# Optimization experiments

Measured on AMD Instinct MI355X. Metric: run time of the kernel, lower is better.

The kernel has to match this reference:

```python
import jax, jax.numpy as jnp
import numpy as np
import math

L, B, S, D, H, FF = 6, 4, 1024, 1024, 16, 4096
HD = D // H
EPS = 1e-5


def _ln(x, g, b):
    m = jnp.mean(x, axis=-1, keepdims=True)
    v = jnp.mean(jnp.square(x - m), axis=-1, keepdims=True)
    return (x - m) / jnp.sqrt(v + EPS) * g + b


def setup_inputs() -> dict:
    key = jax.random.key(0)
    ks = jax.random.split(key, 8)
    std = 0.02
    inp = {
        'x': jax.random.normal(ks[0], (B, S, D), jnp.float32),
        'lengths': jax.random.randint(ks[1], (B,), S // 2, S + 1),
        'rel_bias': jax.random.normal(ks[2], (H, S, S), jnp.float32) * std,
        'ln1_g': jnp.ones((L, D), jnp.float32),
        'ln1_b': jnp.zeros((L, D), jnp.float32),
        'qkv_w': jax.random.normal(ks[3], (L, D, 3 * D), jnp.float32) * std,
        'qkv_b': jnp.zeros((L, 3 * D), jnp.float32),
        'out_w': jax.random.normal(ks[4], (L, D, D), jnp.float32) * std,
        'out_b': jnp.zeros((L, D), jnp.float32),
        'ln2_g': jnp.ones((L, D), jnp.float32),
        'ln2_b': jnp.zeros((L, D), jnp.float32),
        'fc1_w': jax.random.normal(ks[5], (L, D, FF), jnp.float32) * std,
        'fc1_b': jnp.zeros((L, FF), jnp.float32),
        'fc2_w': jax.random.normal(ks[6], (L, FF, D), jnp.float32) * std,
        'fc2_b': jnp.zeros((L, D), jnp.float32),
    }
    return inp


def reference(x, lengths, rel_bias, ln1_g, ln1_b, qkv_w, qkv_b, out_w, out_b,
              ln2_g, ln2_b, fc1_w, fc1_b, fc2_w, fc2_b):
    # causal additive mask [S,S]: -inf above the diagonal (torch.triu diagonal=1)
    ar = jnp.arange(S)
    causal = jnp.where(ar[None, :] > ar[:, None], -jnp.inf, 0.0).astype(x.dtype)
    # key padding mask [B,S]: True where position is padding
    pad = ar[None, :] >= lengths[:, None]
    scale = 1.0 / math.sqrt(HD)

    for i in range(L):
        # --- attention sub-block (pre-LN) ---
        xn = _ln(x, ln1_g[i], ln1_b[i])
        qkv = xn @ qkv_w[i] + qkv_b[i]                      # [B,S,3D]
        q, k, v = jnp.split(qkv, 3, axis=-1)
        q = q.reshape(B, S, H, HD)
        k = k.reshape(B, S, H, HD)
        v = v.reshape(B, S, H, HD)
        scores = jnp.einsum('bqhd,bkhd->bhqk', q, k) * scale  # [B,H,S,S]
        scores = scores + rel_bias[None] + causal[None, None]
        scores = jnp.where(pad[:, None, None, :], -jnp.inf, scores)
        attn = jax.nn.softmax(scores, axis=-1)
        o = jnp.einsum('bhqk,bkhd->bqhd', attn, v).reshape(B, S, D)
        o = o @ out_w[i] + out_b[i]
        o = jnp.where(pad[:, :, None], 0.0, o)
        x = x + o
        # --- feed-forward sub-block (LN inside FF, residual outside) ---
        h = _ln(x, ln2_g[i], ln2_b[i])
        h = jax.nn.gelu(h @ fc1_w[i] + fc1_b[i], approximate=False)
        h = h @ fc2_w[i] + fc2_b[i]
        x = x + h
    return x
```

## Files before the change

kernel.cpp:

```cpp
#include <hip/hip_runtime.h>
#include <cstdint>
#include <cstddef>

constexpr int L_ = 6, B_ = 4, S_ = 1024, D_ = 1024, H_ = 16, FF_ = 4096;
constexpr int D3_ = 3 * D_;
constexpr int HD_ = D_ / H_;

typedef float f32x4 __attribute__((ext_vector_type(4)));
typedef __bf16 bf16x8 __attribute__((ext_vector_type(8)));
typedef unsigned short u16;
typedef u16 u16x4 __attribute__((ext_vector_type(4)));
typedef u16 u16x8 __attribute__((ext_vector_type(8)));

__device__ __forceinline__ u16 f2bf(float f) {
    union { float f; uint32_t u; } v; v.f = f;
    uint32_t r = v.u + 0x7FFFu + ((v.u >> 16) & 1u);
    return (u16)(r >> 16);
}
__device__ __forceinline__ float bf2f(u16 u) {
    union { uint32_t u; float f; } v; v.u = ((uint32_t)u) << 16;
    return v.f;
}

__device__ __forceinline__ void gload16(const void* g, void* l) {
    __builtin_amdgcn_global_load_lds(
        (const __attribute__((address_space(1))) unsigned int*)g,
        (__attribute__((address_space(3))) unsigned int*)l,
        16, 0, 0);
}

__global__ __launch_bounds__(256) void cvt_bias(
    const float* __restrict__ src, u16* __restrict__ dst)
{
    size_t i = ((size_t)blockIdx.x * 256 + threadIdx.x) * 8;
    f32x4 a = *(const f32x4*)(src + i);
    f32x4 b = *(const f32x4*)(src + i + 4);
    u16x8 o;
    #pragma unroll
    for (int r = 0; r < 4; ++r) { o[r] = f2bf(a[r]); o[4 + r] = f2bf(b[r]); }
    *(u16x8*)(dst + i) = o;
}

__global__ __launch_bounds__(256) void cvt_layer(
    const float* __restrict__ qw, const float* __restrict__ ow,
    const float* __restrict__ f1w, const float* __restrict__ f2w,
    u16* __restrict__ tq, u16* __restrict__ to,
    u16* __restrict__ t1, u16* __restrict__ t2)
{
    __shared__ float tile[64][65];
    const int bid = blockIdx.x, tid = threadIdx.x;
    const float* W; u16* WT; int K, N, bn, bk;
    if (bid < 768)       { W = qw;  WT = tq; K = 1024; N = 3072; int t = bid;        bn = (t % 48) * 64; bk = (t / 48) * 64; }
    else if (bid < 1024) { W = ow;  WT = to; K = 1024; N = 1024; int t = bid - 768;  bn = (t % 16) * 64; bk = (t / 16) * 64; }
    else if (bid < 2048) { W = f1w; WT = t1; K = 1024; N = 4096; int t = bid - 1024; bn = (t % 64) * 64; bk = (t / 64) * 64; }
    else                 { W = f2w; WT = t2; K = 4096; N = 1024; int t = bid - 2048; bn = (t % 16) * 64; bk = (t / 16) * 64; }
    #pragma unroll
    for (int i = 0; i < 16; ++i) {
        int idx = i * 256 + tid;
        int r = idx >> 6, c = idx & 63;
        tile[r][c] = W[(size_t)(bk + r) * N + bn + c];
    }
    __syncthreads();
    #pragma unroll
    for (int i = 0; i < 16; ++i) {
        int idx = i * 256 + tid;
        int r = idx >> 6, c = idx & 63;
        WT[(size_t)(bn + r) * K + bk + c] = f2bf(tile[c][r]);
    }
}

__global__ __launch_bounds__(256) void ln_kernel(
    const float* __restrict__ X, const float* __restrict__ g,
    const float* __restrict__ bp, u16* __restrict__ out)
{
    const int row = blockIdx.x, tid = threadIdx.x;
    const float* xr = X + (size_t)row * D_;
    f32x4 v = *(const f32x4*)(xr + tid * 4);
    float s  = v[0] + v[1] + v[2] + v[3];
    float s2 = v[0]*v[0] + v[1]*v[1] + v[2]*v[2] + v[3]*v[3];
    #pragma unroll
    for (int off = 32; off >= 1; off >>= 1) {
        s  += __shfl_down(s,  off);
        s2 += __shfl_down(s2, off);
    }
    __shared__ float red[8];
    const int lane = tid & 63, wid = tid >> 6;
    if (lane == 0) { red[wid] = s; red[4 + wid] = s2; }
    __syncthreads();
    s  = red[0] + red[1] + red[2] + red[3];
    s2 = red[4] + red[5] + red[6] + red[7];
    float mean = s * (1.f / D_);
    float var  = s2 * (1.f / D_) - mean * mean;
    float rstd = rsqrtf(var + 1e-5f);
    f32x4 gv = *(const f32x4*)(g  + tid * 4);
    f32x4 bv = *(const f32x4*)(bp + tid * 4);
    u16x4 o4;
    #pragma unroll
    for (int r = 0; r < 4; ++r) o4[r] = f2bf((v[r] - mean) * rstd * gv[r] + bv[r]);
    *(u16x4*)(out + (size_t)row * D_ + tid * 4) = o4;
}

template<int MODE>
__global__ __launch_bounds__(256, 2) void gemmk(
    const u16* __restrict__ A, const u16* __restrict__ BT,
    const float* __restrict__ bias,
    u16* __restrict__ Cb, float* __restrict__ X, u16* __restrict__ VT,
    const int* __restrict__ lengths,
    int M, int N, int K)
{
    __shared__ __align__(16) char sb0[24576];
    __shared__ __align__(16) char sb1[24576];
    __shared__ __align__(16) char sb2[24576];

    const int tid = threadIdx.x;
    const int lane = tid & 63;
    const int w = tid >> 6;
    const int grp = lane >> 4, l15 = lane & 15;
    const int wm = w >> 1, wn = w & 1;

    const int gx = gridDim.x, gy = gridDim.y;
    const int nwg = gx * gy * gridDim.z;
    int lid = blockIdx.x + gx * (blockIdx.y + gy * blockIdx.z);
    {
        int q = nwg >> 3, r = nwg & 7;
        int xcd = lid & 7, wi = lid >> 3;
        lid = (xcd < r ? xcd * (q + 1) : r * (q + 1) + (xcd - r) * q) + wi;
    }
    const int bx = lid % gx;
    const int byz = lid / gx;
    const int by = byz % gy, bz = byz / gy;

    const int m0 = by * 256, n0 = bx * 128;
    const int Kh = K / gridDim.z;
    const int k0 = bz * Kh;
    const int NT = Kh >> 5;

    const int lrow = lane >> 2;
    const int cchunk = (lane & 3) ^ ((lane >> 3) & 3);
    const u16* gA = A  + (size_t)(m0 + w * 64 + lrow) * K + k0 + cchunk * 8;
    const u16* gB = BT + (size_t)(n0 + w * 32 + lrow) * K + k0 + cchunk * 8;
    const size_t row16 = (size_t)16 * K;
    const int rslot = (grp ^ ((l15 >> 1) & 3)) * 16;

#define STAGE(t, BUF) do {                                                    \
        const u16* pa_ = gA + (size_t)(t) * 32;                               \
        const u16* pb_ = gB + (size_t)(t) * 32;                               \
        char* la_ = (BUF) + w * 4096;                                         \
        char* lb_ = (BUF) + 16384 + w * 2048;                                 \
        gload16(pa_,              la_);                                       \
        gload16(pa_ + row16,      la_ + 1024);                                \
        gload16(pa_ + 2 * row16,  la_ + 2048);                                \
        gload16(pa_ + 3 * row16,  la_ + 3072);                                \
        gload16(pb_,              lb_);                                       \
        gload16(pb_ + row16,      lb_ + 1024); } while (0)

    f32x4 acc[8][4] = {};

    STAGE(0, sb0);
    if (NT > 1) STAGE(1, sb1);
    char* bA = sb0; char* bB = sb1; char* bC = sb2;

    for (int t = 0; t < NT; ++t) {
        if (t + 1 < NT) asm volatile("s_waitcnt vmcnt(6)" ::: "memory");
        else            asm volatile("s_waitcnt vmcnt(0)" ::: "memory");
        __builtin_amdgcn_s_barrier();
        if (t + 2 < NT) STAGE(t + 2, bC);

        const char* Ab = bA;
        const char* Bb = bA + 16384;
        bf16x8 bfr[4], af[8];
        #pragma unroll
        for (int nf = 0; nf < 4; ++nf)
            bfr[nf] = *(const bf16x8*)(Bb + (wn * 64 + nf * 16 + l15) * 64 + rslot);
        #pragma unroll
        for (int mf = 0; mf < 8; ++mf)
            af[mf] = *(const bf16x8*)(Ab + (wm * 128 + mf * 16 + l15) * 64 + rslot);
        __builtin_amdgcn_s_setprio(1);
        #pragma unroll
        for (int mf = 0; mf < 8; ++mf)
            #pragma unroll
            for (int nf = 0; nf < 4; ++nf)
                acc[mf][nf] = __builtin_amdgcn_mfma_f32_16x16x32_bf16(
                    af[mf], bfr[nf], acc[mf][nf], 0, 0, 0);
        __builtin_amdgcn_s_setprio(0);

        char* tmp = bA; bA = bB; bB = bC; bC = tmp;
    }
#undef STAGE

    const float bscale = (k0 == 0) ? 1.f : 0.f;
    #pragma unroll
    for (int mi = 0; mi < 8; ++mi) {
        int row_g = m0 + wm * 128 + mi * 16 + grp * 4;
        #pragma unroll
        for (int nf = 0; nf < 4; ++nf) {
            int col_g = n0 + wn * 64 + nf * 16 + l15;
            float bv = bias[col_g] * bscale;
            f32x4 v = acc[mi][nf];
            if constexpr (MODE == 0) {
                if (col_g < 2 * D_) {
                    #pragma unroll
                    for (int r = 0; r < 4; ++r)
                        Cb[(size_t)(row_g + r) * N + col_g] = f2bf(v[r] + bv);
                } else {
                    u16x4 o4;
                    #pragma unroll
                    for (int r = 0; r < 4; ++r) o4[r] = f2bf(v[r] + bv);
                    int vrow = ((row_g >> 10) << 10) + (col_g - 2 * D_);
                    *(u16x4*)(VT + (size_t)vrow * S_ + (row_g & 1023)) = o4;
                }
            } else if constexpr (MODE == 2) {
                #pragma unroll
                for (int r = 0; r < 4; ++r) {
                    float tv = v[r] + bv;
                    float ge = 0.5f * tv * (1.f + erff(tv * 0.70710678118654752f));
                    Cb[(size_t)(row_g + r) * N + col_g] = f2bf(ge);
                }
            } else if constexpr (MODE == 1) {
                int len = lengths[row_g >> 10];
                #pragma unroll
                for (int r = 0; r < 4; ++r) {
                    int row = row_g + r;
                    float add = ((row & 1023) >= len) ? 0.f : (v[r] + bv);
                    atomicAdd(&X[(size_t)row * N + col_g], add);
                }
            } else {
                #pragma unroll
                for (int r = 0; r < 4; ++r)
                    atomicAdd(&X[(size_t)(row_g + r) * N + col_g], v[r] + bv);
            }
        }
    }
}

__global__ __launch_bounds__(256) void attn_kernel(
    const u16* __restrict__ qkv,
    const u16* __restrict__ vt,
    const u16* __restrict__ rbb,
    const int* __restrict__ lengths,
    u16* __restrict__ obuf)
{
    __shared__ __align__(16) char kls[64 * 128];
    __shared__ __align__(16) char vls[64 * 128];
    const int tid = threadIdx.x, lane = tid & 63, wid = tid >> 6;
    const int grp = lane >> 4, l15 = lane & 15;
    const int bh = blockIdx.x, qt = blockIdx.y;
    const int b = bh >> 4, h = bh & 15;
    const int len = lengths[b];
    const int qrow = qt * 64 + wid * 16 + l15;

    bf16x8 qf[2];
    {
        const u16* qp = qkv + ((size_t)(b * S_ + qrow)) * D3_ + h * 64 + grp * 8;
        qf[0] = *(const bf16x8*)qp;
        qf[1] = *(const bf16x8*)(qp + 32);
    }
    f32x4 oacc[4] = {};
    float m_run = -INFINITY, lsum = 0.f;
    int kt_end = (len + 63) >> 6;
    if (qt + 1 < kt_end) kt_end = qt + 1;

    for (int kt = 0; kt < kt_end; ++kt) {
        __syncthreads();
        #pragma unroll
        for (int i = 0; i < 2; ++i) {
            int id2 = tid + i * 256;
            int r = id2 >> 3, gg = id2 & 7;
            int sw = (r & 7) << 4;
            bf16x8 kv = *(const bf16x8*)(qkv + ((size_t)(b * S_ + kt * 64 + r)) * D3_ + D_ + h * 64 + gg * 8);
            *(bf16x8*)(kls + r * 128 + ((gg * 16) ^ sw)) = kv;
            bf16x8 vv = *(const bf16x8*)(vt + ((size_t)(bh * 64 + r)) * S_ + kt * 64 + gg * 8);
            *(bf16x8*)(vls + r * 128 + ((gg * 16) ^ sw)) = vv;
        }
        __syncthreads();

        f32x4 sf[4] = {};
        #pragma unroll
        for (int f = 0; f < 4; ++f) {
            int r = f * 16 + l15;
            int sw = (r & 7) << 4;
            #pragma unroll
            for (int t = 0; t < 2; ++t) {
                bf16x8 af = *(const bf16x8*)(kls + r * 128 + (((t * 32 + grp * 8) * 2) ^ sw));
                sf[f] = __builtin_amdgcn_mfma_f32_16x16x32_bf16(af, qf[t], sf[f], 0, 0, 0);
            }
        }
        float p[4][4];
        float tmax = -INFINITY;
        #pragma unroll
        for (int f = 0; f < 4; ++f) {
            u16x4 bi = *(const u16x4*)(rbb + ((size_t)h * S_ + qrow) * S_ + kt * 64 + f * 16 + grp * 4);
            #pragma unroll
            for (int r = 0; r < 4; ++r) {
                int kp = kt * 64 + f * 16 + grp * 4 + r;
                bool valid = (kp <= qrow) && (kp < len);
                float sv = valid ? fmaf(sf[f][r], 0.125f, bf2f(bi[r])) : -INFINITY;
                p[f][r] = sv;
                tmax = fmaxf(tmax, sv);
            }
        }
        tmax = fmaxf(tmax, __shfl_xor(tmax, 16));
        tmax = fmaxf(tmax, __shfl_xor(tmax, 32));
        float m_new = fmaxf(m_run, tmax);
        float alpha = expf(m_run - m_new);
        float psum = 0.f;
        #pragma unroll
        for (int f = 0; f < 4; ++f)
            #pragma unroll
            for (int r = 0; r < 4; ++r) {
                float e = expf(p[f][r] - m_new);
                p[f][r] = e; psum += e;
            }
        psum += __shfl_xor(psum, 16);
        psum += __shfl_xor(psum, 32);
        lsum = lsum * alpha + psum;
        m_run = m_new;
        #pragma unroll
        for (int fo = 0; fo < 4; ++fo) {
            oacc[fo][0] *= alpha; oacc[fo][1] *= alpha;
            oacc[fo][2] *= alpha; oacc[fo][3] *= alpha;
        }
        #pragma unroll
        for (int t = 0; t < 2; ++t) {
            union { u16 u[8]; bf16x8 v; } pb;
            #pragma unroll
            for (int j = 0; j < 4; ++j) {
                pb.u[j]     = f2bf(p[2 * t][j]);
                pb.u[4 + j] = f2bf(p[2 * t + 1][j]);
            }
            #pragma unroll
            for (int fo = 0; fo < 4; ++fo) {
                int r = fo * 16 + l15;
                int sw = (r & 7) << 4;
                union { u16x4 h4[2]; bf16x8 v; } av;
                av.h4[0] = *(const u16x4*)(vls + r * 128 + ((t * 64 + grp * 8)      ^ sw));
                av.h4[1] = *(const u16x4*)(vls + r * 128 + ((t * 64 + grp * 8 + 32) ^ sw));
                oacc[fo] = __builtin_amdgcn_mfma_f32_16x16x32_bf16(av.v, pb.v, oacc[fo], 0, 0, 0);
            }
        }
    }
    float inv = 1.f / lsum;
    #pragma unroll
    for (int fo = 0; fo < 4; ++fo)
        #pragma unroll
        for (int r = 0; r < 4; ++r) {
            int hd = fo * 16 + grp * 4 + r;
            obuf[((size_t)(b * S_) + qrow) * D_ + h * 64 + hd] = f2bf(oacc[fo][r] * inv);
        }
}

extern "C" void kernel_launch(void* const* d_in, const int* in_sizes, int n_in,
                              void* d_out, int out_size, void* d_ws, size_t ws_size,
                              hipStream_t stream)
{
    const float* x_in     = (const float*)d_in[0];
    const int*   lengths  = (const int*)d_in[1];
    const float* rel_bias = (const float*)d_in[2];
    const float* ln1_g    = (const float*)d_in[3];
    const float* ln1_b    = (const float*)d_in[4];
    const float* qkv_w    = (const float*)d_in[5];
    const float* qkv_b    = (const float*)d_in[6];
    const float* out_w    = (const float*)d_in[7];
    const float* out_b    = (const float*)d_in[8];
    const float* ln2_g    = (const float*)d_in[9];
    const float* ln2_b    = (const float*)d_in[10];
    const float* fc1_w    = (const float*)d_in[11];
    const float* fc1_b    = (const float*)d_in[12];
    const float* fc2_w    = (const float*)d_in[13];
    const float* fc2_b    = (const float*)d_in[14];
    float* X = (float*)d_out;

    char* ws = (char*)d_ws;
    size_t off = 0;
    auto alloc = [&](size_t bytes) {
        char* p = ws + off;
        off = (off + bytes + 255) & ~(size_t)255;
        return p;
    };
    u16* wT_qkv = (u16*)alloc((size_t)D3_ * D_ * 2);
    u16* wT_out = (u16*)alloc((size_t)D_ * D_ * 2);
    u16* wT_fc1 = (u16*)alloc((size_t)FF_ * D_ * 2);
    u16* wT_fc2 = (u16*)alloc((size_t)D_ * FF_ * 2);
    u16* xn     = (u16*)alloc((size_t)B_ * S_ * D_ * 2);
    u16* qkvb   = (u16*)alloc((size_t)B_ * S_ * D3_ * 2);
    u16* vtb    = (u16*)alloc((size_t)B_ * H_ * HD_ * S_ * 2);
    u16* ob     = (u16*)alloc((size_t)B_ * S_ * D_ * 2);
    u16* h1     = (u16*)alloc((size_t)B_ * S_ * FF_ * 2);
    u16* rbb    = (u16*)alloc((size_t)H_ * S_ * S_ * 2);

    const int M = B_ * S_;

    hipMemcpyAsync(X, x_in, (size_t)M * D_ * sizeof(float),
                   hipMemcpyDeviceToDevice, stream);
    cvt_bias<<<(H_ * S_ * S_) / (256 * 8), 256, 0, stream>>>(rel_bias, rbb);

    for (int i = 0; i < L_; ++i) {
        cvt_layer<<<3072, 256, 0, stream>>>(
            qkv_w + (size_t)i * D_ * D3_, out_w + (size_t)i * D_ * D_,
            fc1_w + (size_t)i * D_ * FF_, fc2_w + (size_t)i * FF_ * D_,
            wT_qkv, wT_out, wT_fc1, wT_fc2);

        ln_kernel<<<M, 256, 0, stream>>>(X, ln1_g + i * D_, ln1_b + i * D_, xn);
        gemmk<0><<<dim3(D3_ / 128, M / 256, 1), 256, 0, stream>>>(
            xn, wT_qkv, qkv_b + (size_t)i * D3_, qkvb, nullptr, vtb, nullptr, M, D3_, D_);
        attn_kernel<<<dim3(B_ * H_, S_ / 64), 256, 0, stream>>>(
            qkvb, vtb, rbb, lengths, ob);
        gemmk<1><<<dim3(D_ / 128, M / 256, 4), 256, 0, stream>>>(
            ob, wT_out, out_b + (size_t)i * D_, nullptr, X, nullptr, lengths, M, D_, D_);

        ln_kernel<<<M, 256, 0, stream>>>(X, ln2_g + i * D_, ln2_b + i * D_, xn);
        gemmk<2><<<dim3(FF_ / 128, M / 256, 1), 256, 0, stream>>>(
            xn, wT_fc1, fc1_b + (size_t)i * FF_, h1, nullptr, nullptr, nullptr, M, FF_, D_);
        gemmk<3><<<dim3(D_ / 128, M / 256, 4), 256, 0, stream>>>(
            h1, wT_fc2, fc2_b + (size_t)i * D_, nullptr, X, nullptr, nullptr, M, D_, FF_);
    }
}
```

Before: 1.962 ms.

## Replace triple-buffered 256x128 GEMM with single-buffer 128x128 tile kernel

Swaps the 256x128 GEMM, which used a triple-buffered LDS pipeline and async gloads, for a simpler 128x128 tile kernel. The new kernel loads one K-slice per iteration with two syncthreads barriers and has no prefetch. Grid sizes change to match, and the out-projection split-K drops from 4 to 2. The aim is more workgroups per GEMM, but the change gives up load/compute overlap and halves per-tile data reuse.

```diff
diff --git a/kernel.cpp b/kernel.cpp
--- a/kernel.cpp
+++ b/kernel.cpp
@@ -101,22 +101,20 @@
 }
 
 template<int MODE>
-__global__ __launch_bounds__(256, 2) void gemmk(
+__global__ __launch_bounds__(256) void gemm128(
     const u16* __restrict__ A, const u16* __restrict__ BT,
     const float* __restrict__ bias,
     u16* __restrict__ Cb, float* __restrict__ X, u16* __restrict__ VT,
     const int* __restrict__ lengths,
     int M, int N, int K)
 {
-    __shared__ __align__(16) char sb0[24576];
-    __shared__ __align__(16) char sb1[24576];
-    __shared__ __align__(16) char sb2[24576];
-
+    __shared__ __align__(16) u16 lA[128 * 32];
+    __shared__ __align__(16) u16 lB[128 * 32];
     const int tid = threadIdx.x;
     const int lane = tid & 63;
-    const int w = tid >> 6;
     const int grp = lane >> 4, l15 = lane & 15;
-    const int wm = w >> 1, wn = w & 1;
+    const int wid = tid >> 6;
+    const int wm = wid >> 1, wn = wid & 1;
 
     const int gx = gridDim.x, gy = gridDim.y;
     const int nwg = gx * gy * gridDim.z;
@@ -130,73 +128,55 @@
     const int byz = lid / gx;
     const int by = byz % gy, bz = byz / gy;
 
-    const int m0 = by * 256, n0 = bx * 128;
+    const int m0 = by * 128, n0 = bx * 128;
     const int Kh = K / gridDim.z;
     const int k0 = bz * Kh;
-    const int NT = Kh >> 5;
 
     const int lrow = lane >> 2;
     const int cchunk = (lane & 3) ^ ((lane >> 3) & 3);
-    const u16* gA = A  + (size_t)(m0 + w * 64 + lrow) * K + k0 + cchunk * 8;
-    const u16* gB = BT + (size_t)(n0 + w * 32 + lrow) * K + k0 + cchunk * 8;
-    const size_t row16 = (size_t)16 * K;
+    const u16* gA = A  + (size_t)(m0 + wid * 32 + lrow) * K + k0 + cchunk * 8;
+    const u16* gB = BT + (size_t)(n0 + wid * 32 + lrow) * K + k0 + cchunk * 8;
+    char* lAw = (char*)lA + wid * 2048;
+    char* lBw = (char*)lB + wid * 2048;
+    const size_t rstep = (size_t)16 * K;
+
     const int rslot = (grp ^ ((l15 >> 1) & 3)) * 16;
 
-#define STAGE(t, BUF) do {                                                    \
-        const u16* pa_ = gA + (size_t)(t) * 32;                               \
-        const u16* pb_ = gB + (size_t)(t) * 32;                               \
-        char* la_ = (BUF) + w * 4096;                                         \
-        char* lb_ = (BUF) + 16384 + w * 2048;                                 \
-        gload16(pa_,              la_);                                       \
-        gload16(pa_ + row16,      la_ + 1024);                                \
-        gload16(pa_ + 2 * row16,  la_ + 2048);                                \
-        gload16(pa_ + 3 * row16,  la_ + 3072);                                \
-        gload16(pb_,              lb_);                                       \
-        gload16(pb_ + row16,      lb_ + 1024); } while (0)
-
-    f32x4 acc[8][4] = {};
-
-    STAGE(0, sb0);
-    if (NT > 1) STAGE(1, sb1);
-    char* bA = sb0; char* bB = sb1; char* bC = sb2;
-
-    for (int t = 0; t < NT; ++t) {
-        if (t + 1 < NT) asm volatile("s_waitcnt vmcnt(6)" ::: "memory");
-        else            asm volatile("s_waitcnt vmcnt(0)" ::: "memory");
-        __builtin_amdgcn_s_barrier();
-        if (t + 2 < NT) STAGE(t + 2, bC);
-
-        const char* Ab = bA;
-        const char* Bb = bA + 16384;
-        bf16x8 bfr[4], af[8];
-        #pragma unroll
-        for (int nf = 0; nf < 4; ++nf)
-            bfr[nf] = *(const bf16x8*)(Bb + (wn * 64 + nf * 16 + l15) * 64 + rslot);
-        #pragma unroll
-        for (int mf = 0; mf < 8; ++mf)
-            af[mf] = *(const bf16x8*)(Ab + (wm * 128 + mf * 16 + l15) * 64 + rslot);
-        __builtin_amdgcn_s_setprio(1);
-        #pragma unroll
-        for (int mf = 0; mf < 8; ++mf)
+    f32x4 acc[4][4] = {};
+    for (int kk = 0; kk < Kh; kk += 32) {
+        gload16(gA + kk,         lAw);
+        gload16(gA + kk + rstep, lAw + 1024);
+        gload16(gB + kk,         lBw);
+        gload16(gB + kk + rstep, lBw + 1024);
+        __syncthreads();
+        bf16x8 af[4], bfr[4];
+        #pragma unroll
+        for (int mf = 0; mf < 4; ++mf) {
+            int r = wm * 64 + mf * 16 + l15;
+            af[mf] = *(const bf16x8*)((const char*)lA + r * 64 + rslot);
+        }
+        #pragma unroll
+        for (int nf = 0; nf < 4; ++nf) {
+            int r = wn * 64 + nf * 16 + l15;
+            bfr[nf] = *(const bf16x8*)((const char*)lB + r * 64 + rslot);
+        }
+        #pragma unroll
+        for (int mf = 0; mf < 4; ++mf)
             #pragma unroll
             for (int nf = 0; nf < 4; ++nf)
-                acc[mf][nf] = __builtin_amdgcn_mfma_f32_16x16x32_bf16(
-                    af[mf], bfr[nf], acc[mf][nf], 0, 0, 0);
-        __builtin_amdgcn_s_setprio(0);
-
-        char* tmp = bA; bA = bB; bB = bC; bC = tmp;
-    }
-#undef STAGE
+                acc[mf][nf] = __builtin_amdgcn_mfma_f32_16x16x32_bf16(af[mf], bfr[nf], acc[mf][nf], 0, 0, 0);
+        __syncthreads();
+    }
 
     const float bscale = (k0 == 0) ? 1.f : 0.f;
     #pragma unroll
-    for (int mi = 0; mi < 8; ++mi) {
-        int row_g = m0 + wm * 128 + mi * 16 + grp * 4;
+    for (int mf = 0; mf < 4; ++mf) {
+        int row_g = m0 + wm * 64 + mf * 16 + grp * 4;
         #pragma unroll
         for (int nf = 0; nf < 4; ++nf) {
             int col_g = n0 + wn * 64 + nf * 16 + l15;
             float bv = bias[col_g] * bscale;
-            f32x4 v = acc[mi][nf];
+            f32x4 v = acc[mf][nf];
             if constexpr (MODE == 0) {
                 if (col_g < 2 * D_) {
                     #pragma unroll
@@ -212,8 +192,8 @@
             } else if constexpr (MODE == 2) {
                 #pragma unroll
                 for (int r = 0; r < 4; ++r) {
-                    float tv = v[r] + bv;
-                    float ge = 0.5f * tv * (1.f + erff(tv * 0.70710678118654752f));
+                    float t = v[r] + bv;
+                    float ge = 0.5f * t * (1.f + erff(t * 0.70710678118654752f));
                     Cb[(size_t)(row_g + r) * N + col_g] = f2bf(ge);
                 }
             } else if constexpr (MODE == 1) {
@@ -401,17 +381,17 @@
             wT_qkv, wT_out, wT_fc1, wT_fc2);
 
         ln_kernel<<<M, 256, 0, stream>>>(X, ln1_g + i * D_, ln1_b + i * D_, xn);
-        gemmk<0><<<dim3(D3_ / 128, M / 256, 1), 256, 0, stream>>>(
+        gemm128<0><<<dim3(D3_ / 128, M / 128, 1), 256, 0, stream>>>(
             xn, wT_qkv, qkv_b + (size_t)i * D3_, qkvb, nullptr, vtb, nullptr, M, D3_, D_);
         attn_kernel<<<dim3(B_ * H_, S_ / 64), 256, 0, stream>>>(
             qkvb, vtb, rbb, lengths, ob);
-        gemmk<1><<<dim3(D_ / 128, M / 256, 4), 256, 0, stream>>>(
+        gemm128<1><<<dim3(D_ / 128, M / 128, 2), 256, 0, stream>>>(
             ob, wT_out, out_b + (size_t)i * D_, nullptr, X, nullptr, lengths, M, D_, D_);
 
         ln_kernel<<<M, 256, 0, stream>>>(X, ln2_g + i * D_, ln2_b + i * D_, xn);
-        gemmk<2><<<dim3(FF_ / 128, M / 256, 1), 256, 0, stream>>>(
+        gemm128<2><<<dim3(FF_ / 128, M / 128, 1), 256, 0, stream>>>(
             xn, wT_fc1, fc1_b + (size_t)i * FF_, h1, nullptr, nullptr, nullptr, M, FF_, D_);
-        gemmk<3><<<dim3(D_ / 128, M / 256, 4), 256, 0, stream>>>(
+        gemm128<3><<<dim3(D_ / 128, M / 128, 4), 256, 0, stream>>>(
             h1, wT_fc2, fc2_b + (size_t)i * D_, nullptr, X, nullptr, nullptr, M, D_, FF_);
     }
 }
```

After: 1.941 ms. No clear change (-1.1%).
